# Performance work log

Hardware: AMD Instinct MI355X
Metric: run time of the kernel (lower is better)

The kernel has to match this reference:

```python
import jax, jax.numpy as jnp
import numpy as np

CD_W = 0.2  # chamfer_weight
EPS = 1e-7


def setup_inputs() -> dict:
    key = jax.random.key(0)
    k1, k2, k3, k4, k5 = jax.random.split(key, 5)
    B, N, K = 16, 4096, 4096
    num_add, obj_num_p = 8, 512
    return {
        "adv_pc": jax.random.normal(k1, (B, N, 3), dtype=jnp.float32),
        "ori_pc": jax.random.normal(k2, (B, K, 3), dtype=jnp.float32),
        "adv_obj": jax.random.normal(k3, (B, num_add, obj_num_p, 3), dtype=jnp.float32),
        "ori_obj": jax.random.normal(k4, (B, num_add, obj_num_p, 3), dtype=jnp.float32),
        "weights": jax.random.uniform(k5, (B,), dtype=jnp.float32),
    }


def reference(adv_pc, ori_pc, adv_obj, ori_obj, weights):
    B = adv_pc.shape[0]
    # --- Chamfer (method='adv2ori'): mean over adv points of min squared dist to ori ---
    a2 = jnp.sum(adv_pc * adv_pc, axis=-1)            # [B, N]
    o2 = jnp.sum(ori_pc * ori_pc, axis=-1)            # [B, K]
    cross = jnp.einsum('bnd,bkd->bnk', adv_pc, ori_pc)  # [B, N, K]
    sqdist = a2[:, :, None] + o2[:, None, :] - 2.0 * cross  # [B, N, K]
    loss1 = jnp.mean(jnp.min(sqdist, axis=2), axis=1)  # [B] adv->ori NN sq dist
    chamfer_loss = jnp.mean(loss1 * weights)
    # --- Global L2 dist between flattened adv/ori objects ---
    diff = adv_obj.reshape(B, -1, 3) - ori_obj.reshape(B, -1, 3)
    l2 = jnp.sqrt(jnp.sum(diff * diff, axis=(1, 2)) + EPS)  # [B]
    l2_loss = jnp.mean(l2 * weights)
    return l2_loss + CD_W * chamfer_loss
```

## Files before the change

kernel.cpp:

```cpp
#include <hip/hip_runtime.h>
#include <math.h>

typedef short bf16x8 __attribute__((ext_vector_type(8)));
typedef float f32x16 __attribute__((ext_vector_type(16)));
typedef unsigned int u32x4 __attribute__((ext_vector_type(4)));

#define B 16
#define N 4096
#define K 4096
#define OBJ_ELEMS (8*512*3)
#define OBJ_VEC4  (OBJ_ELEMS/4)
#define NSEG 32
#define NCHUNK (N/NSEG)
#define BLK 512
#define OBJ_V4_PER_BLK (OBJ_VEC4/NSEG)
#define CD_W 0.2f
#define EPS_F 1e-7f

#define CS_OFF 0
#define LS_OFF (B*NSEG)

#define MIN3(a,b,c) fminf(fminf((a),(b)),(c))

__device__ __forceinline__ unsigned int cvt_pk_bf16(float lo, float hi) {
    unsigned int r;
    asm volatile("v_cvt_pk_bf16_f32 %0, %1, %2" : "=v"(r) : "v"(lo), "v"(hi));
    return r;
}

__global__ __launch_bounds__(BLK, 4) void chamfer_mfma_kernel(
    const float* __restrict__ adv, const float* __restrict__ ori,
    const float* __restrict__ adv_obj, const float* __restrict__ ori_obj,
    float* __restrict__ csum, float* __restrict__ lsq)
{
    __shared__ uint2 slds[K];
    __shared__ float rowmin[8][32];
    __shared__ float red_c[2], red_l[2];

    const int nseg = blockIdx.x;
    const int b    = blockIdx.y;
    const int tid  = threadIdx.x;
    const int wid  = tid >> 6;
    const int lane = tid & 63;
    const int col  = lane & 31;
    const int hi   = lane >> 5;
    const int rg   = wid & 3;
    const int kh   = wid >> 2;

    {
        const float4* src =
            reinterpret_cast<const float4*>(ori + (size_t)(b*K + tid*8)*3);
        float4 f0 = src[0], f1 = src[1], f2 = src[2];
        float4 f3 = src[3], f4 = src[4], f5 = src[5];
        float xs[8], ys[8], zs[8];
        xs[0]=f0.x; ys[0]=f0.y; zs[0]=f0.z;
        xs[1]=f0.w; ys[1]=f1.x; zs[1]=f1.y;
        xs[2]=f1.z; ys[2]=f1.w; zs[2]=f2.x;
        xs[3]=f2.y; ys[3]=f2.z; zs[3]=f2.w;
        xs[4]=f3.x; ys[4]=f3.y; zs[4]=f3.z;
        xs[5]=f3.w; ys[5]=f4.x; zs[5]=f4.y;
        xs[6]=f4.z; ys[6]=f4.w; zs[6]=f5.x;
        xs[7]=f5.y; ys[7]=f5.z; zs[7]=f5.w;
        #pragma unroll
        for (int j = 0; j < 8; ++j) {
            float x = xs[j], y = ys[j], z = zs[j];
            float o2 = x*x + y*y + z*z;
            uint2 e;
            e.x = cvt_pk_bf16(-2.f*x, -2.f*y);
            e.y = cvt_pk_bf16(-2.f*z, o2);
            slds[tid*8 + j] = e;
        }
    }

    const int n = nseg*NCHUNK + rg*32 + col;
    const float* ap = adv + (size_t)(b*N + n)*3;
    float ax = ap[0], ay = ap[1], az = ap[2];
    float a2 = ax*ax + ay*ay + az*az;
    unsigned int a01 = 0u, a23 = 0u;
    if (hi == 0) {
        a01 = cvt_pk_bf16(ax, ay);
        a23 = cvt_pk_bf16(az, 1.0f);
    }
    u32x4 aw = {a01, a23, 0u, 0u};
    bf16x8 bfrag = __builtin_bit_cast(bf16x8, aw);

    __syncthreads();

    float m = INFINITY;
    const f32x16 zc = {0,0,0,0, 0,0,0,0, 0,0,0,0, 0,0,0,0};
    const float4* s4 = reinterpret_cast<const float4*>(slds);

    #pragma unroll
    for (int ph = 0; ph < 4; ++ph) {
        float4 f[8];
        #pragma unroll
        for (int j = 0; j < 8; ++j)
            f[j] = s4[(kh*32 + ph*8 + j)*32 + col];
        #pragma unroll
        for (int j = 0; j < 8; ++j) {
            u32x4 uu = __builtin_bit_cast(u32x4, f[j]);
            u32x4 w0 = {uu.x, uu.y, 0u, 0u};
            u32x4 w1 = {uu.z, uu.w, 0u, 0u};
            bf16x8 t0 = __builtin_bit_cast(bf16x8, w0);
            bf16x8 t1 = __builtin_bit_cast(bf16x8, w1);
            f32x16 c0 = __builtin_amdgcn_mfma_f32_32x32x16_bf16(t0, bfrag, zc, 0,0,0);
            f32x16 c1 = __builtin_amdgcn_mfma_f32_32x32x16_bf16(t1, bfrag, zc, 0,0,0);
            #define V(i) ((i) < 16 ? c0[(i)] : c1[(i)-16])
            float g0 = MIN3(V(0),  V(1),  V(2));
            float g1 = MIN3(V(3),  V(4),  V(5));
            float g2 = MIN3(V(6),  V(7),  V(8));
            float g3 = MIN3(V(9),  V(10), V(11));
            float g4 = MIN3(V(12), V(13), V(14));
            float g5 = MIN3(V(15), V(16), V(17));
            float g6 = MIN3(V(18), V(19), V(20));
            float g7 = MIN3(V(21), V(22), V(23));
            float g8 = MIN3(V(24), V(25), V(26));
            float g9 = MIN3(V(27), V(28), V(29));
            float h0 = MIN3(g0, g1, g2);
            float h1 = MIN3(g3, g4, g5);
            float h2 = MIN3(g6, g7, g8);
            float h3 = MIN3(g9, V(30), V(31));
            m = MIN3(MIN3(h0, h1, h2), h3, m);
            #undef V
        }
    }

    m = fminf(m, __shfl_xor(m, 32));
    m += a2;
    if (hi == 0) rowmin[wid][col] = m;
    __syncthreads();

    float s = 0.f;
    if (wid < 2) {
        int row = tid;
        int rg2 = row >> 5, ri = row & 31;
        s = fminf(rowmin[rg2][ri], rowmin[4 + rg2][ri]);
    } else if (wid < 4) {
        int li = (wid - 2)*64 + lane;
        if (li < OBJ_V4_PER_BLK) {
            int idx = b*OBJ_VEC4 + nseg*OBJ_V4_PER_BLK + li;
            float4 a = reinterpret_cast<const float4*>(adv_obj)[idx];
            float4 o = reinterpret_cast<const float4*>(ori_obj)[idx];
            float dx = a.x - o.x, dy = a.y - o.y, dz = a.z - o.z, dw = a.w - o.w;
            s = dx*dx + dy*dy + dz*dz + dw*dw;
        }
    }
    #pragma unroll
    for (int off = 32; off; off >>= 1) s += __shfl_down(s, off);
    if (lane == 0) {
        if (wid < 2)       red_c[wid]     = s;
        else if (wid < 4)  red_l[wid - 2] = s;
    }
    __syncthreads();
    if (tid == 0) csum[b*NSEG + nseg] = red_c[0] + red_c[1];
    if (tid == 1) lsq [b*NSEG + nseg] = red_l[0] + red_l[1];
}

__global__ __launch_bounds__(256) void final_kernel(
    const float* __restrict__ csum, const float* __restrict__ lsq,
    const float* __restrict__ w, float* __restrict__ out)
{
    const int tid = threadIdx.x;
    float c = csum[2*tid] + csum[2*tid + 1];
    float l = lsq [2*tid] + lsq [2*tid + 1];
    #pragma unroll
    for (int off = 8; off; off >>= 1) {
        c += __shfl_down(c, off, 16);
        l += __shfl_down(l, off, 16);
    }
    __shared__ float sc[B], sl[B];
    int bb = tid >> 4;
    if ((tid & 15) == 0) { sc[bb] = c; sl[bb] = l; }
    __syncthreads();
    if (tid < 64) {
        float cc = 0.f, ll = 0.f;
        if (tid < B) {
            float wt = w[tid];
            cc = (sc[tid] / (float)N) * wt;
            ll = sqrtf(sl[tid] + EPS_F) * wt;
        }
        #pragma unroll
        for (int off = 8; off; off >>= 1) {
            cc += __shfl_down(cc, off);
            ll += __shfl_down(ll, off);
        }
        if (tid == 0) out[0] = ll / (float)B + CD_W * (cc / (float)B);
    }
}

extern "C" void kernel_launch(void* const* d_in, const int* in_sizes, int n_in,
                              void* d_out, int out_size, void* d_ws, size_t ws_size,
                              hipStream_t stream)
{
    const float* adv_pc  = (const float*)d_in[0];
    const float* ori_pc  = (const float*)d_in[1];
    const float* adv_obj = (const float*)d_in[2];
    const float* ori_obj = (const float*)d_in[3];
    const float* weights = (const float*)d_in[4];
    float* out = (float*)d_out;
    float* ws  = (float*)d_ws;

    float* csum = ws + CS_OFF;
    float* lsq  = ws + LS_OFF;

    chamfer_mfma_kernel<<<dim3(NSEG, B), dim3(BLK), 0, stream>>>(
        adv_pc, ori_pc, adv_obj, ori_obj, csum, lsq);

    final_kernel<<<dim3(1), dim3(256), 0, stream>>>(csum, lsq, weights, out);
}
```

Measured before the change: 16.71 us.

## Split work so each wave handles two adv row tiles, reusing LDS fragments

Each wave now covers 64 adv points (two B fragments) over a quarter of the K range, where before it covered 32 adv points over half of K. Every LDS fragment load now feeds four MFMAs instead of two, halving LDS reads per MFMA. The final reduction merges four partial row-mins instead of two. This costs more live registers for two accumulator pairs and adds one more cross-wave min stage.

```diff
diff --git a/kernel.cpp b/kernel.cpp
--- a/kernel.cpp
+++ b/kernel.cpp
@@ -28,13 +28,34 @@
     return r;
 }
 
+__device__ __forceinline__ float tree32(const f32x16& c0, const f32x16& c1,
+                                        float m) {
+    #define V(i) ((i) < 16 ? c0[(i)] : c1[(i)-16])
+    float g0 = MIN3(V(0),  V(1),  V(2));
+    float g1 = MIN3(V(3),  V(4),  V(5));
+    float g2 = MIN3(V(6),  V(7),  V(8));
+    float g3 = MIN3(V(9),  V(10), V(11));
+    float g4 = MIN3(V(12), V(13), V(14));
+    float g5 = MIN3(V(15), V(16), V(17));
+    float g6 = MIN3(V(18), V(19), V(20));
+    float g7 = MIN3(V(21), V(22), V(23));
+    float g8 = MIN3(V(24), V(25), V(26));
+    float g9 = MIN3(V(27), V(28), V(29));
+    float h0 = MIN3(g0, g1, g2);
+    float h1 = MIN3(g3, g4, g5);
+    float h2 = MIN3(g6, g7, g8);
+    float h3 = MIN3(g9, V(30), V(31));
+    return MIN3(MIN3(h0, h1, h2), h3, m);
+    #undef V
+}
+
 __global__ __launch_bounds__(BLK, 4) void chamfer_mfma_kernel(
     const float* __restrict__ adv, const float* __restrict__ ori,
     const float* __restrict__ adv_obj, const float* __restrict__ ori_obj,
     float* __restrict__ csum, float* __restrict__ lsq)
 {
     __shared__ uint2 slds[K];
-    __shared__ float rowmin[8][32];
+    __shared__ float rowmin[8][64];
     __shared__ float red_c[2], red_l[2];
 
     const int nseg = blockIdx.x;
@@ -44,8 +65,8 @@
     const int lane = tid & 63;
     const int col  = lane & 31;
     const int hi   = lane >> 5;
-    const int rg   = wid & 3;
-    const int kh   = wid >> 2;
+    const int rg   = wid & 1;
+    const int kh   = wid >> 1;
 
     {
         const float4* src =
@@ -72,69 +93,61 @@
         }
     }
 
-    const int n = nseg*NCHUNK + rg*32 + col;
-    const float* ap = adv + (size_t)(b*N + n)*3;
-    float ax = ap[0], ay = ap[1], az = ap[2];
-    float a2 = ax*ax + ay*ay + az*az;
-    unsigned int a01 = 0u, a23 = 0u;
+    const int n0 = nseg*NCHUNK + rg*64 + col;
+    const float* ap0 = adv + (size_t)(b*N + n0)*3;
+    const float* ap1 = ap0 + 32*3;
+    float ax0 = ap0[0], ay0 = ap0[1], az0 = ap0[2];
+    float ax1 = ap1[0], ay1 = ap1[1], az1 = ap1[2];
+    float a2_0 = ax0*ax0 + ay0*ay0 + az0*az0;
+    float a2_1 = ax1*ax1 + ay1*ay1 + az1*az1;
+    unsigned int b00 = 0u, b01 = 0u, b10 = 0u, b11 = 0u;
     if (hi == 0) {
-        a01 = cvt_pk_bf16(ax, ay);
-        a23 = cvt_pk_bf16(az, 1.0f);
-    }
-    u32x4 aw = {a01, a23, 0u, 0u};
-    bf16x8 bfrag = __builtin_bit_cast(bf16x8, aw);
-
-    __syncthreads();
-
-    float m = INFINITY;
+        b00 = cvt_pk_bf16(ax0, ay0);
+        b01 = cvt_pk_bf16(az0, 1.0f);
+        b10 = cvt_pk_bf16(ax1, ay1);
+        b11 = cvt_pk_bf16(az1, 1.0f);
+    }
+    u32x4 bw0 = {b00, b01, 0u, 0u};
+    u32x4 bw1 = {b10, b11, 0u, 0u};
+    bf16x8 bfrag0 = __builtin_bit_cast(bf16x8, bw0);
+    bf16x8 bfrag1 = __builtin_bit_cast(bf16x8, bw1);
+
+    __syncthreads();
+
+    float m0 = INFINITY, m1 = INFINITY;
     const f32x16 zc = {0,0,0,0, 0,0,0,0, 0,0,0,0, 0,0,0,0};
     const float4* s4 = reinterpret_cast<const float4*>(slds);
 
-    #pragma unroll
-    for (int ph = 0; ph < 4; ++ph) {
-        float4 f[8];
-        #pragma unroll
-        for (int j = 0; j < 8; ++j)
-            f[j] = s4[(kh*32 + ph*8 + j)*32 + col];
-        #pragma unroll
-        for (int j = 0; j < 8; ++j) {
-            u32x4 uu = __builtin_bit_cast(u32x4, f[j]);
-            u32x4 w0 = {uu.x, uu.y, 0u, 0u};
-            u32x4 w1 = {uu.z, uu.w, 0u, 0u};
-            bf16x8 t0 = __builtin_bit_cast(bf16x8, w0);
-            bf16x8 t1 = __builtin_bit_cast(bf16x8, w1);
-            f32x16 c0 = __builtin_amdgcn_mfma_f32_32x32x16_bf16(t0, bfrag, zc, 0,0,0);
-            f32x16 c1 = __builtin_amdgcn_mfma_f32_32x32x16_bf16(t1, bfrag, zc, 0,0,0);
-            #define V(i) ((i) < 16 ? c0[(i)] : c1[(i)-16])
-            float g0 = MIN3(V(0),  V(1),  V(2));
-            float g1 = MIN3(V(3),  V(4),  V(5));
-            float g2 = MIN3(V(6),  V(7),  V(8));
-            float g3 = MIN3(V(9),  V(10), V(11));
-            float g4 = MIN3(V(12), V(13), V(14));
-            float g5 = MIN3(V(15), V(16), V(17));
-            float g6 = MIN3(V(18), V(19), V(20));
-            float g7 = MIN3(V(21), V(22), V(23));
-            float g8 = MIN3(V(24), V(25), V(26));
-            float g9 = MIN3(V(27), V(28), V(29));
-            float h0 = MIN3(g0, g1, g2);
-            float h1 = MIN3(g3, g4, g5);
-            float h2 = MIN3(g6, g7, g8);
-            float h3 = MIN3(g9, V(30), V(31));
-            m = MIN3(MIN3(h0, h1, h2), h3, m);
-            #undef V
-        }
-    }
-
-    m = fminf(m, __shfl_xor(m, 32));
-    m += a2;
-    if (hi == 0) rowmin[wid][col] = m;
+    #pragma unroll 4
+    for (int t = kh*16; t < kh*16 + 16; ++t) {
+        float4 q = s4[t*32 + col];
+        u32x4 uu = __builtin_bit_cast(u32x4, q);
+        u32x4 w0 = {uu.x, uu.y, 0u, 0u};
+        u32x4 w1 = {uu.z, uu.w, 0u, 0u};
+        bf16x8 t0 = __builtin_bit_cast(bf16x8, w0);
+        bf16x8 t1 = __builtin_bit_cast(bf16x8, w1);
+        f32x16 c0 = __builtin_amdgcn_mfma_f32_32x32x16_bf16(t0, bfrag0, zc, 0,0,0);
+        f32x16 c1 = __builtin_amdgcn_mfma_f32_32x32x16_bf16(t1, bfrag0, zc, 0,0,0);
+        f32x16 c2 = __builtin_amdgcn_mfma_f32_32x32x16_bf16(t0, bfrag1, zc, 0,0,0);
+        f32x16 c3 = __builtin_amdgcn_mfma_f32_32x32x16_bf16(t1, bfrag1, zc, 0,0,0);
+        m0 = tree32(c0, c1, m0);
+        m1 = tree32(c2, c3, m1);
+    }
+
+    m0 = fminf(m0, __shfl_xor(m0, 32)) + a2_0;
+    m1 = fminf(m1, __shfl_xor(m1, 32)) + a2_1;
+    if (hi == 0) {
+        rowmin[wid][col]      = m0;
+        rowmin[wid][32 + col] = m1;
+    }
     __syncthreads();
 
     float s = 0.f;
     if (wid < 2) {
         int row = tid;
-        int rg2 = row >> 5, ri = row & 31;
-        s = fminf(rowmin[rg2][ri], rowmin[4 + rg2][ri]);
+        int rg2 = row >> 6, ri = row & 63;
+        s = fminf(fminf(rowmin[rg2][ri],     rowmin[2 + rg2][ri]),
+                  fminf(rowmin[4 + rg2][ri], rowmin[6 + rg2][ri]));
     } else if (wid < 4) {
         int li = (wid - 2)*64 + lane;
         if (li < OBJ_V4_PER_BLK) {
```

After: 16.67 us. Within noise of the previous version (-0.2%).
